# Kernel tuning notes

Measured on AMD Instinct MI355X. Metric: run time of the kernel, lower is better.

The kernel has to match this reference:

```python
import jax, jax.numpy as jnp
import numpy as np

N, B1, B2 = 16384, 1024, 64           # instances, level-1 bags, level-2 bags
C1, C2, K, P = 32, 64, 5, 2           # conv filters, kernel, pool size
D = 4 * 4 * C2                        # flatten dim: 28->24->12->8->4 spatial
ATT, CLS = 256, 512                   # attention units, classifier units


def _conv_relu(x, w, b):
    y = jax.lax.conv_general_dilated(
        x, w, window_strides=(1, 1), padding='VALID',
        dimension_numbers=('NHWC', 'HWIO', 'NHWC'))
    return jax.nn.relu(y + b)


def _maxpool(x):
    return jax.lax.reduce_window(
        x, -jnp.inf, jax.lax.max, (1, P, P, 1), (1, P, P, 1), 'VALID')


def _att_weights(emb, W, b, v, vb):
    # Dense(tanh) -> Dropout(identity at inference) -> Dense(1, sigmoid),
    # then GLOBAL softmax over all rows (softmax of the transposed [1,n] vector).
    h = jnp.tanh(emb @ W + b)
    s = jax.nn.sigmoid(h @ v + vb)     # [n, 1]
    return jax.nn.softmax(s[:, 0])     # [n], softmax across ALL rows


def setup_inputs() -> dict:
    key = jax.random.key(0)
    ks = jax.random.split(key, 12)

    def g(k, shape, scale=0.05):
        return scale * jax.random.normal(k, shape, dtype=jnp.float32)

    return {
        'x': jax.random.normal(ks[0], (N, 28, 28, 1), dtype=jnp.float32),
        'conv1_w': g(ks[1], (K, K, 1, C1)),
        'conv1_b': jnp.zeros((C1,), jnp.float32),
        'conv2_w': g(ks[2], (K, K, C1, C2)),
        'conv2_b': jnp.zeros((C2,), jnp.float32),
        'att1_W': g(ks[3], (D, ATT)), 'att1_b': jnp.zeros((ATT,), jnp.float32),
        'att1_v': g(ks[4], (ATT, 1)), 'att1_vb': jnp.zeros((1,), jnp.float32),
        'att2_W': g(ks[5], (D, ATT)), 'att2_b': jnp.zeros((ATT,), jnp.float32),
        'att2_v': g(ks[6], (ATT, 1)), 'att2_vb': jnp.zeros((1,), jnp.float32),
        'att3_W': g(ks[7], (D, ATT)), 'att3_b': jnp.zeros((ATT,), jnp.float32),
        'att3_v': g(ks[8], (ATT, 1)), 'att3_vb': jnp.zeros((1,), jnp.float32),
        'cls_W': g(ks[9], (D, CLS)), 'cls_b': jnp.zeros((CLS,), jnp.float32),
        'out_W': g(ks[10], (CLS, 1)), 'out_b': jnp.zeros((1,), jnp.float32),
        # sorted contiguous bag ids, every bag present (matches unique_with_counts loop)
        'first_lab': jnp.repeat(jnp.arange(B1, dtype=jnp.int32), N // B1),
        'second_lab': jnp.repeat(jnp.arange(B2, dtype=jnp.int32), B1 // B2),
    }


def reference(x, conv1_w, conv1_b, conv2_w, conv2_b,
              att1_W, att1_b, att1_v, att1_vb,
              att2_W, att2_b, att2_v, att2_vb,
              att3_W, att3_b, att3_v, att3_vb,
              cls_W, cls_b, out_W, out_b,
              first_lab, second_lab):
    h = _maxpool(_conv_relu(x, conv1_w, conv1_b))
    h = _maxpool(_conv_relu(h, conv2_w, conv2_b))       # [N, 4, 4, C2]
    emb1 = h.reshape(h.shape[0], -1)                    # [N, D]

    # level 1: attention-weighted bag pooling (instances -> B1 bags)
    w1 = _att_weights(emb1, att1_W, att1_b, att1_v, att1_vb)          # [N]
    emb2 = jax.ops.segment_sum(w1[:, None] * emb1, first_lab,
                               num_segments=B1)                       # [B1, D]

    # level 2: B1 bags -> B2 bags
    w2 = _att_weights(emb2, att2_W, att2_b, att2_v, att2_vb)          # [B1]
    emb3 = jax.ops.segment_sum(w2[:, None] * emb2, second_lab,
                               num_segments=B2)                       # [B2, D]

    # level 3: single outer bag over all B2 bags
    w3 = _att_weights(emb3, att3_W, att3_b, att3_v, att3_vb)          # [B2]
    outer = w3[None, :] @ emb3                                        # [1, D]

    pred = jax.nn.sigmoid((outer @ cls_W + cls_b) @ out_W + out_b)    # [1, 1]
    return pred
```

## Files before the change

kernel.cpp:

```cpp
#include <hip/hip_runtime.h>
#include <hip/hip_bf16.h>
#include <math.h>

typedef float f32x4 __attribute__((ext_vector_type(4)));
using bf16x8 = __attribute__((ext_vector_type(8))) short;
using f32x16 = __attribute__((ext_vector_type(16))) float;
typedef unsigned short ushortT;
using u16x4 = __attribute__((ext_vector_type(4))) unsigned short;

__device__ __forceinline__ ushortT f2bf(float f) {
  unsigned int u = __builtin_bit_cast(unsigned int, f);
  u = (u + 0x7FFFu + ((u >> 16) & 1u)) >> 16;
  return (ushortT)u;
}
__device__ __forceinline__ float bf2f(ushortT u) {
  return __builtin_bit_cast(float, (unsigned int)u << 16);
}
__device__ __forceinline__ void gload_lds16(const void* gsrc, void* ldst) {
  __builtin_amdgcn_global_load_lds(
      (const __attribute__((address_space(1))) unsigned int*)gsrc,
      (__attribute__((address_space(3))) unsigned int*)ldst, 16, 0, 0);
}

__global__ __launch_bounds__(256) void prepack_kernel(
    const float* __restrict__ w1, const float* __restrict__ w2,
    const float* __restrict__ aW1, const float* __restrict__ aW2,
    const float* __restrict__ aW3, const float* __restrict__ cls_W,
    const float* __restrict__ out_W, ushortT* __restrict__ Bp1,
    ushortT* __restrict__ Bp2, ushortT* __restrict__ BpA1,
    ushortT* __restrict__ BpA2, ushortT* __restrict__ BpA3,
    float* __restrict__ u) {
  const int i = blockIdx.x * 256 + threadIdx.x;
  const int n1 = 1024, n2 = 51200, nA = 262144, nU = 65536;
  if (i < n1) {
    int nt = i >> 9, l = (i >> 3) & 63, j = i & 7;
    int tap = ((l >> 4) << 3) + j, ch = nt * 16 + (l & 15);
    Bp1[i] = (tap < 25) ? f2bf(w1[tap * 32 + ch]) : (ushortT)0;
  } else if (i < n1 + n2) {
    int t = i - n1;
    int s = t >> 10, r = t & 1023;
    int nt = r >> 9, l = (r >> 3) & 63, j = r & 7;
    int k = s * 16 + ((l >> 5) << 3) + j, co = nt * 32 + (l & 31);
    Bp2[t] = f2bf(w2[k * 64 + co]);
  } else if (i < n1 + n2 + 3 * nA) {
    int t = i - n1 - n2;
    int m = t >> 18, r0 = t & (nA - 1);
    const float* aW = (m == 0) ? aW1 : ((m == 1) ? aW2 : aW3);
    ushortT* dst = (m == 0) ? BpA1 : ((m == 1) ? BpA2 : BpA3);
    int nt = r0 >> 15, r = r0 & 32767;
    int s = r >> 9, l = (r >> 3) & 63, j = r & 7;
    int k = s * 16 + ((l >> 5) << 3) + j, col = nt * 32 + (l & 31);
    dst[r0] = f2bf(aW[k * 256 + col]);
  } else if (i < n1 + n2 + 3 * nA + nU) {
    int t = i - (n1 + n2 + 3 * nA);
    int k = t >> 6, lane = t & 63;
    float p = 0.f;
#pragma unroll
    for (int j = 0; j < 8; ++j) {
      int jj = lane + j * 64;
      p += cls_W[k * 512 + jj] * out_W[jj];
    }
#pragma unroll
    for (int off = 32; off; off >>= 1) p += __shfl_xor(p, off, 64);
    if (lane == 0) u[k] = p;
  }
}

#define PADW 40
__global__ __launch_bounds__(256, 2) void fused_conv_mfma_kernel(
    const float* __restrict__ x, const ushortT* __restrict__ Bp1,
    const float* __restrict__ b1g, const ushortT* __restrict__ Bp2,
    const float* __restrict__ b2g, ushortT* __restrict__ emb1) {
  __shared__ ushortT xs[4][784];
  __shared__ ushortT h1s[4][144 * PADW];
  __shared__ ushortT Bbuf[2][4096];

  const int tid = threadIdx.x, wv = tid >> 6, lane = tid & 63;
  const int inst = blockIdx.x * 4 + wv;

  {
    int base = wv * 2048;
    gload_lds16((const char*)Bp2 + base + lane * 16, (char*)&Bbuf[0][0] + base);
    gload_lds16((const char*)Bp2 + base + 1024 + lane * 16,
                (char*)&Bbuf[0][0] + base + 1024);
  }

  const float* xg = x + (size_t)inst * 784;
  for (int i = lane; i < 784; i += 64) xs[wv][i] = f2bf(xg[i]);
  __syncthreads();

  {
    const int arow = lane & 15, kg = lane >> 4;
    int koff[8], kval[8];
#pragma unroll
    for (int j = 0; j < 8; ++j) {
      int tap = kg * 8 + j;
      int ky = (tap * 13) >> 6;
      int kx = tap - ky * 5;
      kval[j] = (tap < 25);
      koff[j] = kval[j] ? (ky * 28 + kx) : 0;
    }
    bf16x8 w1f0 = *(const bf16x8*)&Bp1[lane * 8];
    bf16x8 w1f1 = *(const bf16x8*)&Bp1[(64 + lane) * 8];
    const float bA = b1g[arow], bB = b1g[16 + arow];

#pragma unroll 4
    for (int g = 0; g < 36; ++g) {
      int R = g * 16 + arow;
      int q = R >> 2, quad = R & 3;
      int qy = q / 12, qx = q - qy * 12;
      int base = (2 * qy + (quad >> 1)) * 28 + 2 * qx + (quad & 1);
      bf16x8 a;
#pragma unroll
      for (int j = 0; j < 8; ++j) {
        ushortT vv = xs[wv][base + koff[j]];
        a[j] = (short)(kval[j] ? vv : (ushortT)0);
      }
      f32x4 c0, c1;
#pragma unroll
      for (int z = 0; z < 4; ++z) { c0[z] = 0.f; c1[z] = 0.f; }
      c0 = __builtin_amdgcn_mfma_f32_16x16x32_bf16(a, w1f0, c0, 0, 0, 0);
      c1 = __builtin_amdgcn_mfma_f32_16x16x32_bf16(a, w1f1, c1, 0, 0, 0);
      int qo = g * 4 + kg;
      float m0 = fmaxf(fmaxf(c0[0], c0[1]), fmaxf(c0[2], c0[3]));
      float m1 = fmaxf(fmaxf(c1[0], c1[1]), fmaxf(c1[2], c1[3]));
      h1s[wv][qo * PADW + arow] = f2bf(fmaxf(m0 + bA, 0.f));
      h1s[wv][qo * PADW + 16 + arow] = f2bf(fmaxf(m1 + bB, 0.f));
    }
  }
  __syncthreads();

  {
    const int hi = lane >> 5, l31 = lane & 31;
    int rowbase0, rowbase1;
    {
      int q2 = l31 >> 2, quad2 = l31 & 3;
      rowbase0 = (2 * (q2 >> 2) + (quad2 >> 1)) * 12 + 2 * (q2 & 3) + (quad2 & 1);
      q2 = (32 + l31) >> 2;
      rowbase1 = (2 * (q2 >> 2) + (quad2 >> 1)) * 12 + 2 * (q2 & 3) + (quad2 & 1);
    }
    const ushortT* h1w = &h1s[wv][0];

    f32x16 a00, a01, a10, a11;
#pragma unroll
    for (int z = 0; z < 16; ++z) { a00[z] = 0.f; a01[z] = 0.f; a10[z] = 0.f; a11[z] = 0.f; }

    for (int c = 0; c < 13; ++c) {
      if (c < 12) {
        char* dstb = (char*)&Bbuf[(c + 1) & 1][0];
        const char* srcb = (const char*)Bp2 + (size_t)(c + 1) * 8192;
        if (c + 1 < 12) {
          gload_lds16(srcb + wv * 2048 + lane * 16, dstb + wv * 2048);
          gload_lds16(srcb + wv * 2048 + 1024 + lane * 16,
                      dstb + wv * 2048 + 1024);
        } else {
          gload_lds16(srcb + wv * 1024 + lane * 16, dstb + wv * 1024);
        }
      }
      const ushortT* bb = &Bbuf[c & 1][0];
      const int ns = (c < 12) ? 4 : 2;
#pragma unroll
      for (int i = 0; i < 4; ++i) {
        if (i < ns) {
          int s = c * 4 + i;
          int tap = s >> 1;
          int ky = (tap * 13) >> 6, kx = tap - ky * 5;
          int aoff = (ky * 12 + kx) * PADW + ((s & 1) << 4) + hi * 8;
          bf16x8 af0 = *(const bf16x8*)&h1w[rowbase0 * PADW + aoff];
          bf16x8 af1 = *(const bf16x8*)&h1w[rowbase1 * PADW + aoff];
          bf16x8 bf0 = *(const bf16x8*)&bb[i * 1024 + lane * 8];
          bf16x8 bf1 = *(const bf16x8*)&bb[i * 1024 + 512 + lane * 8];
          a00 = __builtin_amdgcn_mfma_f32_32x32x16_bf16(af0, bf0, a00, 0, 0, 0);
          a01 = __builtin_amdgcn_mfma_f32_32x32x16_bf16(af0, bf1, a01, 0, 0, 0);
          a10 = __builtin_amdgcn_mfma_f32_32x32x16_bf16(af1, bf0, a10, 0, 0, 0);
          a11 = __builtin_amdgcn_mfma_f32_32x32x16_bf16(af1, bf1, a11, 0, 0, 0);
        }
      }
      __syncthreads();
    }

    const float b2_0 = b2g[l31], b2_1 = b2g[32 + l31];
    ushortT* erow = emb1 + (size_t)inst * 1024;
#pragma unroll
    for (int rg = 0; rg < 4; ++rg) {
      float m00 = fmaxf(fmaxf(a00[rg * 4], a00[rg * 4 + 1]),
                        fmaxf(a00[rg * 4 + 2], a00[rg * 4 + 3]));
      float m01 = fmaxf(fmaxf(a01[rg * 4], a01[rg * 4 + 1]),
                        fmaxf(a01[rg * 4 + 2], a01[rg * 4 + 3]));
      float m10 = fmaxf(fmaxf(a10[rg * 4], a10[rg * 4 + 1]),
                        fmaxf(a10[rg * 4 + 2], a10[rg * 4 + 3]));
      float m11 = fmaxf(fmaxf(a11[rg * 4], a11[rg * 4 + 1]),
                        fmaxf(a11[rg * 4 + 2], a11[rg * 4 + 3]));
      int p0 = 2 * rg + hi, p1 = 8 + 2 * rg + hi;
      erow[p0 * 64 + l31] = f2bf(fmaxf(m00 + b2_0, 0.f));
      erow[p0 * 64 + 32 + l31] = f2bf(fmaxf(m01 + b2_1, 0.f));
      erow[p1 * 64 + l31] = f2bf(fmaxf(m10 + b2_0, 0.f));
      erow[p1 * 64 + 32 + l31] = f2bf(fmaxf(m11 + b2_1, 0.f));
    }
  }
}

__global__ __launch_bounds__(512) void att_mfma_kernel(
    const ushortT* __restrict__ emb, const ushortT* __restrict__ Bp,
    const float* __restrict__ bias, const float* __restrict__ v,
    const float* __restrict__ vb, float* __restrict__ s_out) {
  __shared__ float part[64][8];
  const int tid = threadIdx.x, wv = tid >> 6, lane = tid & 63;
  const int hi = lane >> 5, l31 = lane & 31;
  const int row0 = blockIdx.x * 64;

  const ushortT* ap0 = emb + (size_t)(row0 + l31) * 1024 + hi * 8;
  const ushortT* ap1 = ap0 + 32 * 1024;
  const ushortT* bp = Bp + ((size_t)wv * 64 * 64 + lane) * 8;

  f32x16 acc0, acc1;
#pragma unroll
  for (int z = 0; z < 16; ++z) { acc0[z] = 0.f; acc1[z] = 0.f; }

#pragma unroll 8
  for (int s = 0; s < 64; ++s) {
    bf16x8 bfr = *(const bf16x8*)(bp + s * 512);
    bf16x8 af0 = *(const bf16x8*)(ap0 + s * 16);
    bf16x8 af1 = *(const bf16x8*)(ap1 + s * 16);
    acc0 = __builtin_amdgcn_mfma_f32_32x32x16_bf16(af0, bfr, acc0, 0, 0, 0);
    acc1 = __builtin_amdgcn_mfma_f32_32x32x16_bf16(af1, bfr, acc1, 0, 0, 0);
  }

  const int col = wv * 32 + l31;
  const float bc = bias[col], vc = v[col];
#pragma unroll
  for (int r = 0; r < 16; ++r) {
    float p = tanhf(acc0[r] + bc) * vc;
#pragma unroll
    for (int off = 16; off >= 1; off >>= 1) p += __shfl_xor(p, off, 64);
    if (l31 == 0) part[(r & 3) + 8 * (r >> 2) + 4 * hi][wv] = p;
  }
#pragma unroll
  for (int r = 0; r < 16; ++r) {
    float p = tanhf(acc1[r] + bc) * vc;
#pragma unroll
    for (int off = 16; off >= 1; off >>= 1) p += __shfl_xor(p, off, 64);
    if (l31 == 0) part[32 + (r & 3) + 8 * (r >> 2) + 4 * hi][wv] = p;
  }
  __syncthreads();
  if (tid < 64) {
    float ssum = vb[0];
#pragma unroll
    for (int w = 0; w < 8; ++w) ssum += part[tid][w];
    s_out[row0 + tid] = 1.f / (1.f + expf(-ssum));
  }
}

__global__ __launch_bounds__(1024) void softmax_reduce_kernel(
    const float* __restrict__ s, int M, float* __restrict__ red) {
  __shared__ float sm[16], ss[16];
  const int tid = threadIdx.x;
  float mx = -INFINITY;
  for (int i = tid; i < M; i += 1024) mx = fmaxf(mx, s[i]);
#pragma unroll
  for (int off = 32; off; off >>= 1) mx = fmaxf(mx, __shfl_xor(mx, off, 64));
  if ((tid & 63) == 0) sm[tid >> 6] = mx;
  __syncthreads();
  float gmax = sm[0];
#pragma unroll
  for (int w = 1; w < 16; ++w) gmax = fmaxf(gmax, sm[w]);
  float sum = 0.f;
  for (int i = tid; i < M; i += 1024) sum += expf(s[i] - gmax);
#pragma unroll
  for (int off = 32; off; off >>= 1) sum += __shfl_xor(sum, off, 64);
  if ((tid & 63) == 0) ss[tid >> 6] = sum;
  __syncthreads();
  if (tid == 0) {
    float t = 0.f;
#pragma unroll
    for (int w = 0; w < 16; ++w) t += ss[w];
    red[0] = gmax;
    red[1] = t;
  }
}

__global__ __launch_bounds__(256) void segsum16_kernel(
    const ushortT* __restrict__ emb_in, const float* __restrict__ s,
    const float* __restrict__ red, ushortT* __restrict__ emb_out) {
  __shared__ float wsh[16];
  const int b = blockIdx.x, tid = threadIdx.x;
  if (tid < 16) wsh[tid] = expf(s[b * 16 + tid] - red[0]) / red[1];
  __syncthreads();
  f32x4 acc;
#pragma unroll
  for (int z = 0; z < 4; ++z) acc[z] = 0.f;
#pragma unroll
  for (int k = 0; k < 16; ++k) {
    u16x4 uu = *(const u16x4*)(emb_in + (size_t)(b * 16 + k) * 1024 + tid * 4);
    float w = wsh[k];
    acc[0] += bf2f(uu[0]) * w;
    acc[1] += bf2f(uu[1]) * w;
    acc[2] += bf2f(uu[2]) * w;
    acc[3] += bf2f(uu[3]) * w;
  }
  u16x4 o;
#pragma unroll
  for (int z = 0; z < 4; ++z) o[z] = f2bf(acc[z]);
  *(u16x4*)(emb_out + (size_t)b * 1024 + tid * 4) = o;
}

__global__ __launch_bounds__(1024) void final_kernel(
    const ushortT* __restrict__ emb3, const float* __restrict__ s3,
    const float* __restrict__ red3, const float* __restrict__ u,
    const float* __restrict__ cls_b, const float* __restrict__ out_W,
    const float* __restrict__ out_b, float* __restrict__ out) {
  __shared__ float w3[64];
  __shared__ float redp[16];
  const int tid = threadIdx.x;
  if (tid < 64) w3[tid] = expf(s3[tid] - red3[0]) / red3[1];
  __syncthreads();
  float outer = 0.f;
#pragma unroll
  for (int b = 0; b < 64; ++b) outer += w3[b] * bf2f(emb3[b * 1024 + tid]);
  float val = outer * u[tid] + ((tid < 512) ? cls_b[tid] * out_W[tid] : 0.f);
#pragma unroll
  for (int off = 32; off; off >>= 1) val += __shfl_xor(val, off, 64);
  if ((tid & 63) == 0) redp[tid >> 6] = val;
  __syncthreads();
  if (tid == 0) {
    float z = out_b[0];
#pragma unroll
    for (int w = 0; w < 16; ++w) z += redp[w];
    out[0] = 1.f / (1.f + expf(-z));
  }
}

extern "C" void kernel_launch(void* const* d_in, const int* in_sizes, int n_in,
                              void* d_out, int out_size, void* d_ws,
                              size_t ws_size, hipStream_t stream) {
  const float* x       = (const float*)d_in[0];
  const float* conv1_w = (const float*)d_in[1];
  const float* conv1_b = (const float*)d_in[2];
  const float* conv2_w = (const float*)d_in[3];
  const float* conv2_b = (const float*)d_in[4];
  const float* att1_W  = (const float*)d_in[5];
  const float* att1_b  = (const float*)d_in[6];
  const float* att1_v  = (const float*)d_in[7];
  const float* att1_vb = (const float*)d_in[8];
  const float* att2_W  = (const float*)d_in[9];
  const float* att2_b  = (const float*)d_in[10];
  const float* att2_v  = (const float*)d_in[11];
  const float* att2_vb = (const float*)d_in[12];
  const float* att3_W  = (const float*)d_in[13];
  const float* att3_b  = (const float*)d_in[14];
  const float* att3_v  = (const float*)d_in[15];
  const float* att3_vb = (const float*)d_in[16];
  const float* cls_W   = (const float*)d_in[17];
  const float* cls_b   = (const float*)d_in[18];
  const float* out_W   = (const float*)d_in[19];
  const float* out_b   = (const float*)d_in[20];

  char* p = (char*)d_ws;
  ushortT* emb1 = (ushortT*)p; p += (size_t)16384 * 1024 * 2;
  ushortT* Bp1  = (ushortT*)p; p += 2048;
  ushortT* Bp2  = (ushortT*)p; p += 102400;
  ushortT* BpA1 = (ushortT*)p; p += 524288;
  ushortT* BpA2 = (ushortT*)p; p += 524288;
  ushortT* BpA3 = (ushortT*)p; p += 524288;
  float* u      = (float*)p;   p += 4096;
  ushortT* emb2 = (ushortT*)p; p += (size_t)1024 * 1024 * 2;
  ushortT* emb3 = (ushortT*)p; p += 64 * 1024 * 2;
  float* s1     = (float*)p;   p += 16384 * 4;
  float* s2     = (float*)p;   p += 4096;
  float* s3     = (float*)p;   p += 256;
  float* red1   = (float*)p;   p += 256;
  float* red2   = (float*)p;   p += 256;
  float* red3   = (float*)p;   p += 256;

  prepack_kernel<<<3532, 256, 0, stream>>>(conv1_w, conv2_w, att1_W, att2_W,
                                           att3_W, cls_W, out_W, Bp1, Bp2,
                                           BpA1, BpA2, BpA3, u);
  fused_conv_mfma_kernel<<<4096, 256, 0, stream>>>(x, Bp1, conv1_b, Bp2,
                                                   conv2_b, emb1);
  att_mfma_kernel<<<256, 512, 0, stream>>>(emb1, BpA1, att1_b, att1_v, att1_vb,
                                           s1);
  softmax_reduce_kernel<<<1, 1024, 0, stream>>>(s1, 16384, red1);
  segsum16_kernel<<<1024, 256, 0, stream>>>(emb1, s1, red1, emb2);
  att_mfma_kernel<<<16, 512, 0, stream>>>(emb2, BpA2, att2_b, att2_v, att2_vb,
                                          s2);
  softmax_reduce_kernel<<<1, 1024, 0, stream>>>(s2, 1024, red2);
  segsum16_kernel<<<64, 256, 0, stream>>>(emb2, s2, red2, emb3);
  att_mfma_kernel<<<1, 512, 0, stream>>>(emb3, BpA3, att3_b, att3_v, att3_vb,
                                         s3);
  softmax_reduce_kernel<<<1, 1024, 0, stream>>>(s3, 64, red3);
  final_kernel<<<1, 1024, 0, stream>>>(emb3, s3, red3, u, cls_b, out_W, out_b,
                                       (float*)d_out);
}
```

Before: 437.7 us.

## Retile embeddings into MFMA-fragment layout and stream conv2 weights from global

Changes the embedding storage to a tiled layout of 32-row groups laid out by k-chunk, so the attention GEMM loads A fragments as contiguous 16-byte lane reads. The segment-sum and final kernels are updated to use the same layout. Conv2 weights are repacked and read straight from global/L2 per step instead of double-buffered into LDS, which removes the per-chunk barriers. LDS use is cut (smaller padding, x buffer shared with the output staging area) so occupancy can rise to 3 blocks. The risks are weight-read latency going through L2 instead of LDS and register pressure from unrolling all 50 steps.

```diff
diff --git a/kernel.cpp b/kernel.cpp
--- a/kernel.cpp
+++ b/kernel.cpp
@@ -16,11 +16,7 @@
 __device__ __forceinline__ float bf2f(ushortT u) {
   return __builtin_bit_cast(float, (unsigned int)u << 16);
 }
-__device__ __forceinline__ void gload_lds16(const void* gsrc, void* ldst) {
-  __builtin_amdgcn_global_load_lds(
-      (const __attribute__((address_space(1))) unsigned int*)gsrc,
-      (__attribute__((address_space(3))) unsigned int*)ldst, 16, 0, 0);
-}
+
 
 __global__ __launch_bounds__(256) void prepack_kernel(
     const float* __restrict__ w1, const float* __restrict__ w2,
@@ -38,19 +34,20 @@
     Bp1[i] = (tap < 25) ? f2bf(w1[tap * 32 + ch]) : (ushortT)0;
   } else if (i < n1 + n2) {
     int t = i - n1;
-    int s = t >> 10, r = t & 1023;
-    int nt = r >> 9, l = (r >> 3) & 63, j = r & 7;
-    int k = s * 16 + ((l >> 5) << 3) + j, co = nt * 32 + (l & 31);
-    Bp2[t] = f2bf(w2[k * 64 + co]);
+    int co = t & 63, k = t >> 6;
+    int s = k >> 4, hi = (k >> 3) & 1, j = k & 7;
+    int nt = co >> 5, l31 = co & 31;
+    Bp2[(s * 2 + nt) * 512 + (hi * 32 + l31) * 8 + j] = f2bf(w2[k * 64 + co]);
   } else if (i < n1 + n2 + 3 * nA) {
     int t = i - n1 - n2;
-    int m = t >> 18, r0 = t & (nA - 1);
+    int m = t >> 18, r = t & (nA - 1);
     const float* aW = (m == 0) ? aW1 : ((m == 1) ? aW2 : aW3);
     ushortT* dst = (m == 0) ? BpA1 : ((m == 1) ? BpA2 : BpA3);
-    int nt = r0 >> 15, r = r0 & 32767;
-    int s = r >> 9, l = (r >> 3) & 63, j = r & 7;
-    int k = s * 16 + ((l >> 5) << 3) + j, col = nt * 32 + (l & 31);
-    dst[r0] = f2bf(aW[k * 256 + col]);
+    int col = r & 255, k = r >> 8;
+    int nt = col >> 5, l31 = col & 31;
+    int s = k >> 4, hi = (k >> 3) & 1, j = k & 7;
+    dst[nt * 32768 + s * 512 + (hi * 32 + l31) * 8 + j] =
+        f2bf(aW[k * 256 + col]);
   } else if (i < n1 + n2 + 3 * nA + nU) {
     int t = i - (n1 + n2 + 3 * nA);
     int k = t >> 6, lane = t & 63;
@@ -66,28 +63,33 @@
   }
 }
 
-#define PADW 40
-__global__ __launch_bounds__(256, 2) void fused_conv_mfma_kernel(
+#define PADW 36
+__global__ __launch_bounds__(256, 3) void fused_conv_mfma_kernel(
     const float* __restrict__ x, const ushortT* __restrict__ Bp1,
     const float* __restrict__ b1g, const ushortT* __restrict__ Bp2,
     const float* __restrict__ b2g, ushortT* __restrict__ emb1) {
-  __shared__ ushortT xs[4][784];
   __shared__ ushortT h1s[4][144 * PADW];
-  __shared__ ushortT Bbuf[2][4096];
+  __shared__ __align__(16) char uni[4 * 2080];
 
   const int tid = threadIdx.x, wv = tid >> 6, lane = tid & 63;
   const int inst = blockIdx.x * 4 + wv;
+  ushortT* xs = (ushortT*)(uni + wv * 2080);
+  ushortT* h1w = &h1s[wv][0];
 
   {
-    int base = wv * 2048;
-    gload_lds16((const char*)Bp2 + base + lane * 16, (char*)&Bbuf[0][0] + base);
-    gload_lds16((const char*)Bp2 + base + 1024 + lane * 16,
-                (char*)&Bbuf[0][0] + base + 1024);
-  }
-
-  const float* xg = x + (size_t)inst * 784;
-  for (int i = lane; i < 784; i += 64) xs[wv][i] = f2bf(xg[i]);
-  __syncthreads();
+    const float* xg = x + (size_t)inst * 784;
+#pragma unroll
+    for (int t = 0; t < 4; ++t) {
+      int g = lane + t * 64;
+      if (g < 196) {
+        f32x4 v = *(const f32x4*)&xg[g * 4];
+        u16x4 o;
+#pragma unroll
+        for (int z = 0; z < 4; ++z) o[z] = f2bf(v[z]);
+        *(u16x4*)&xs[g * 4] = o;
+      }
+    }
+  }
 
   {
     const int arow = lane & 15, kg = lane >> 4;
@@ -113,7 +115,7 @@
       bf16x8 a;
 #pragma unroll
       for (int j = 0; j < 8; ++j) {
-        ushortT vv = xs[wv][base + koff[j]];
+        ushortT vv = xs[base + koff[j]];
         a[j] = (short)(kval[j] ? vv : (ushortT)0);
       }
       f32x4 c0, c1;
@@ -124,11 +126,10 @@
       int qo = g * 4 + kg;
       float m0 = fmaxf(fmaxf(c0[0], c0[1]), fmaxf(c0[2], c0[3]));
       float m1 = fmaxf(fmaxf(c1[0], c1[1]), fmaxf(c1[2], c1[3]));
-      h1s[wv][qo * PADW + arow] = f2bf(fmaxf(m0 + bA, 0.f));
-      h1s[wv][qo * PADW + 16 + arow] = f2bf(fmaxf(m1 + bB, 0.f));
-    }
-  }
-  __syncthreads();
+      h1w[qo * PADW + arow] = f2bf(fmaxf(m0 + bA, 0.f));
+      h1w[qo * PADW + 16 + arow] = f2bf(fmaxf(m1 + bB, 0.f));
+    }
+  }
 
   {
     const int hi = lane >> 5, l31 = lane & 31;
@@ -139,48 +140,31 @@
       q2 = (32 + l31) >> 2;
       rowbase1 = (2 * (q2 >> 2) + (quad2 >> 1)) * 12 + 2 * (q2 & 3) + (quad2 & 1);
     }
-    const ushortT* h1w = &h1s[wv][0];
+    const int ab0 = rowbase0 * PADW + hi * 8;
+    const int ab1 = rowbase1 * PADW + hi * 8;
+    const ushortT* bglane = Bp2 + lane * 8;
 
     f32x16 a00, a01, a10, a11;
 #pragma unroll
     for (int z = 0; z < 16; ++z) { a00[z] = 0.f; a01[z] = 0.f; a10[z] = 0.f; a11[z] = 0.f; }
 
-    for (int c = 0; c < 13; ++c) {
-      if (c < 12) {
-        char* dstb = (char*)&Bbuf[(c + 1) & 1][0];
-        const char* srcb = (const char*)Bp2 + (size_t)(c + 1) * 8192;
-        if (c + 1 < 12) {
-          gload_lds16(srcb + wv * 2048 + lane * 16, dstb + wv * 2048);
-          gload_lds16(srcb + wv * 2048 + 1024 + lane * 16,
-                      dstb + wv * 2048 + 1024);
-        } else {
-          gload_lds16(srcb + wv * 1024 + lane * 16, dstb + wv * 1024);
-        }
-      }
-      const ushortT* bb = &Bbuf[c & 1][0];
-      const int ns = (c < 12) ? 4 : 2;
-#pragma unroll
-      for (int i = 0; i < 4; ++i) {
-        if (i < ns) {
-          int s = c * 4 + i;
-          int tap = s >> 1;
-          int ky = (tap * 13) >> 6, kx = tap - ky * 5;
-          int aoff = (ky * 12 + kx) * PADW + ((s & 1) << 4) + hi * 8;
-          bf16x8 af0 = *(const bf16x8*)&h1w[rowbase0 * PADW + aoff];
-          bf16x8 af1 = *(const bf16x8*)&h1w[rowbase1 * PADW + aoff];
-          bf16x8 bf0 = *(const bf16x8*)&bb[i * 1024 + lane * 8];
-          bf16x8 bf1 = *(const bf16x8*)&bb[i * 1024 + 512 + lane * 8];
-          a00 = __builtin_amdgcn_mfma_f32_32x32x16_bf16(af0, bf0, a00, 0, 0, 0);
-          a01 = __builtin_amdgcn_mfma_f32_32x32x16_bf16(af0, bf1, a01, 0, 0, 0);
-          a10 = __builtin_amdgcn_mfma_f32_32x32x16_bf16(af1, bf0, a10, 0, 0, 0);
-          a11 = __builtin_amdgcn_mfma_f32_32x32x16_bf16(af1, bf1, a11, 0, 0, 0);
-        }
-      }
-      __syncthreads();
-    }
-
+#pragma unroll
+    for (int s = 0; s < 50; ++s) {
+      const int tap = s >> 1;
+      const int ky = tap / 5, kx = tap - (tap / 5) * 5;
+      const int aoff = (ky * 12 + kx) * PADW + ((s & 1) << 4);
+      bf16x8 bf0 = *(const bf16x8*)&bglane[(s * 2 + 0) * 512];
+      bf16x8 bf1 = *(const bf16x8*)&bglane[(s * 2 + 1) * 512];
+      bf16x8 af0 = *(const bf16x8*)&h1w[ab0 + aoff];
+      bf16x8 af1 = *(const bf16x8*)&h1w[ab1 + aoff];
+      a00 = __builtin_amdgcn_mfma_f32_32x32x16_bf16(af0, bf0, a00, 0, 0, 0);
+      a01 = __builtin_amdgcn_mfma_f32_32x32x16_bf16(af0, bf1, a01, 0, 0, 0);
+      a10 = __builtin_amdgcn_mfma_f32_32x32x16_bf16(af1, bf0, a10, 0, 0, 0);
+      a11 = __builtin_amdgcn_mfma_f32_32x32x16_bf16(af1, bf1, a11, 0, 0, 0);
+    }
+
+    ushortT* epi = (ushortT*)(uni + wv * 2080);
     const float b2_0 = b2g[l31], b2_1 = b2g[32 + l31];
-    ushortT* erow = emb1 + (size_t)inst * 1024;
 #pragma unroll
     for (int rg = 0; rg < 4; ++rg) {
       float m00 = fmaxf(fmaxf(a00[rg * 4], a00[rg * 4 + 1]),
@@ -192,10 +176,24 @@
       float m11 = fmaxf(fmaxf(a11[rg * 4], a11[rg * 4 + 1]),
                         fmaxf(a11[rg * 4 + 2], a11[rg * 4 + 3]));
       int p0 = 2 * rg + hi, p1 = 8 + 2 * rg + hi;
-      erow[p0 * 64 + l31] = f2bf(fmaxf(m00 + b2_0, 0.f));
-      erow[p0 * 64 + 32 + l31] = f2bf(fmaxf(m01 + b2_1, 0.f));
-      erow[p1 * 64 + l31] = f2bf(fmaxf(m10 + b2_0, 0.f));
-      erow[p1 * 64 + 32 + l31] = f2bf(fmaxf(m11 + b2_1, 0.f));
+      epi[p0 * 64 + l31] = f2bf(fmaxf(m00 + b2_0, 0.f));
+      epi[p0 * 64 + 32 + l31] = f2bf(fmaxf(m01 + b2_1, 0.f));
+      epi[p1 * 64 + l31] = f2bf(fmaxf(m10 + b2_0, 0.f));
+      epi[p1 * 64 + 32 + l31] = f2bf(fmaxf(m11 + b2_1, 0.f));
+    }
+  }
+  __syncthreads();
+
+  {
+    const int bid = blockIdx.x;
+    ushortT* dstbase = emb1 + (size_t)(bid >> 3) * 32768;
+    const int instoff = 4 * (bid & 7);
+#pragma unroll
+    for (int z = 0; z < 2; ++z) {
+      int kchunk = (tid >> 2) + z * 64;
+      int i = tid & 3;
+      bf16x8 vv = *(const bf16x8*)(uni + i * 2080 + kchunk * 16);
+      *(bf16x8*)&dstbase[(size_t)kchunk * 256 + (instoff + i) * 8] = vv;
     }
   }
 }
@@ -209,8 +207,8 @@
   const int hi = lane >> 5, l31 = lane & 31;
   const int row0 = blockIdx.x * 64;
 
-  const ushortT* ap0 = emb + (size_t)(row0 + l31) * 1024 + hi * 8;
-  const ushortT* ap1 = ap0 + 32 * 1024;
+  const ushortT* ap0 = emb + (size_t)(row0 >> 5) * 32768 + hi * 256 + l31 * 8;
+  const ushortT* ap1 = ap0 + 32768;
   const ushortT* bp = Bp + ((size_t)wv * 64 * 64 + lane) * 8;
 
   f32x16 acc0, acc1;
@@ -220,8 +218,8 @@
 #pragma unroll 8
   for (int s = 0; s < 64; ++s) {
     bf16x8 bfr = *(const bf16x8*)(bp + s * 512);
-    bf16x8 af0 = *(const bf16x8*)(ap0 + s * 16);
-    bf16x8 af1 = *(const bf16x8*)(ap1 + s * 16);
+    bf16x8 af0 = *(const bf16x8*)(ap0 + s * 512);
+    bf16x8 af1 = *(const bf16x8*)(ap1 + s * 512);
     acc0 = __builtin_amdgcn_mfma_f32_32x32x16_bf16(af0, bfr, acc0, 0, 0, 0);
     acc1 = __builtin_amdgcn_mfma_f32_32x32x16_bf16(af1, bfr, acc1, 0, 0, 0);
   }
@@ -286,12 +284,15 @@
   const int b = blockIdx.x, tid = threadIdx.x;
   if (tid < 16) wsh[tid] = expf(s[b * 16 + tid] - red[0]) / red[1];
   __syncthreads();
+  const int kc = tid >> 1, jj = (tid & 1) * 4;
+  const ushortT* src =
+      emb_in + (size_t)(b >> 1) * 32768 + kc * 256 + ((b & 1) * 16) * 8 + jj;
   f32x4 acc;
 #pragma unroll
   for (int z = 0; z < 4; ++z) acc[z] = 0.f;
 #pragma unroll
   for (int k = 0; k < 16; ++k) {
-    u16x4 uu = *(const u16x4*)(emb_in + (size_t)(b * 16 + k) * 1024 + tid * 4);
+    u16x4 uu = *(const u16x4*)(src + k * 8);
     float w = wsh[k];
     acc[0] += bf2f(uu[0]) * w;
     acc[1] += bf2f(uu[1]) * w;
@@ -301,7 +302,8 @@
   u16x4 o;
 #pragma unroll
   for (int z = 0; z < 4; ++z) o[z] = f2bf(acc[z]);
-  *(u16x4*)(emb_out + (size_t)b * 1024 + tid * 4) = o;
+  *(u16x4*)(emb_out + (size_t)(b >> 5) * 32768 + kc * 256 + (b & 31) * 8 + jj) =
+      o;
 }
 
 __global__ __launch_bounds__(1024) void final_kernel(
@@ -314,9 +316,12 @@
   const int tid = threadIdx.x;
   if (tid < 64) w3[tid] = expf(s3[tid] - red3[0]) / red3[1];
   __syncthreads();
+  const int kc = tid >> 3, j = tid & 7;
   float outer = 0.f;
 #pragma unroll
-  for (int b = 0; b < 64; ++b) outer += w3[b] * bf2f(emb3[b * 1024 + tid]);
+  for (int b = 0; b < 64; ++b)
+    outer += w3[b] *
+             bf2f(emb3[(size_t)(b >> 5) * 32768 + kc * 256 + (b & 31) * 8 + j]);
   float val = outer * u[tid] + ((tid < 512) ? cls_b[tid] * out_W[tid] : 0.f);
 #pragma unroll
   for (int off = 32; off; off >>= 1) val += __shfl_xor(val, off, 64);
```

New measurement: 493.2 us. 1.13x slower.
